# Optimization experiments

Hardware: AMD Instinct MI355X
Metric: run time of the kernel (lower is better)

Reference implementation:

```python
import jax, jax.numpy as jnp
import numpy as np

GROUP = 128          # quantization group size along K
ALIGN = 64           # M padding alignment (DeepGEMM, no swap-ab)
FP8_MAX = 448.0      # E4M3 max
EPS = 1e-4
MIN_SCALE = EPS / FP8_MAX


def _quant_per_token_group(a_bf16):
    """Per-token, per-128-group fp8 quantization along K.
    a_bf16: [M, K] bf16 -> (q [M, K] f32 fp8-rounded values, scales [M, K/GROUP] f32)"""
    M, K = a_bf16.shape
    g = a_bf16.astype(jnp.float32).reshape(M, K // GROUP, GROUP)
    amax = jnp.max(jnp.abs(g), axis=-1)                      # [M, K/GROUP]
    scale = jnp.maximum(amax, EPS) / FP8_MAX
    scale = jnp.maximum(scale, MIN_SCALE)                    # torch.clamp(min=...)
    q = jnp.clip(g / scale[..., None], -FP8_MAX, FP8_MAX)
    q = q.astype(jnp.float8_e4m3fn).astype(jnp.float32)      # fp8 rounding
    return q.reshape(M, K), scale


def setup_inputs() -> dict:
    key = jax.random.key(0)
    k1, k2, k3 = jax.random.split(key, 3)
    M, K, N = 8192, 4096, 4096
    inp = jax.random.normal(k1, (M, K), dtype=jnp.bfloat16)
    # weight stored as [N, K], values already fp8-representable (as DeepGEMM expects fp8 weights)
    w = jax.random.normal(k2, (N, K), dtype=jnp.float32)
    w = jnp.clip(w, -FP8_MAX, FP8_MAX).astype(jnp.float8_e4m3fn).astype(jnp.float32)
    # per-128x128-block weight scales, [N/128, K/128], positive
    ws = jax.random.uniform(k3, (N // GROUP, K // GROUP), dtype=jnp.float32,
                            minval=0.005, maxval=0.02)
    return {"input": inp, "weight": w, "weight_scales": ws}


def reference(input, weight, weight_scales):
    M, K = input.shape
    N = weight.shape[0]
    # pad M to multiple of ALIGN with zeros
    target_m = (M + ALIGN - 1) // ALIGN * ALIGN
    x = jnp.pad(input, ((0, target_m - M), (0, 0))) if target_m > M else input
    # fp8 per-token-group quantization of activations
    q, a_scales = _quant_per_token_group(x)                  # [Mp,K], [Mp,K/G]
    # dequantize both operands (the math fp8_gemm_nt computes)
    a_deq = q * jnp.repeat(a_scales, GROUP, axis=1)          # [Mp, K]
    w_deq = weight * jnp.repeat(jnp.repeat(weight_scales, GROUP, axis=0), GROUP, axis=1)  # [N, K]
    out = jnp.einsum('mk,nk->mn', a_deq, w_deq).astype(jnp.bfloat16)
    return out[:M, :]
```

## Files before the change

### kernel.cpp

```cpp
#include <hip/hip_runtime.h>
#include <hip/hip_bf16.h>

typedef unsigned short u16;
typedef unsigned int u32;
typedef __attribute__((ext_vector_type(8))) short short8;
typedef __attribute__((ext_vector_type(4))) float f32x4;

__device__ __forceinline__ u16 bf16_rne(float x) {
  __hip_bfloat16 h = __float2bfloat16(x);
  return __builtin_bit_cast(u16, h);
}

__global__ __launch_bounds__(256) void quant_dequant_a(
    const float* __restrict__ A, u16* __restrict__ AD, int K) {
  const int b = blockIdx.x;
  const int row = b >> 1;
  const int t = threadIdx.x;
  const size_t base = (size_t)row * K + (size_t)(b & 1) * 2048 + (size_t)t * 8;

  float4 v0 = *(const float4*)(A + base);
  float4 v1 = *(const float4*)(A + base + 4);
  float f[8] = {v0.x, v0.y, v0.z, v0.w, v1.x, v1.y, v1.z, v1.w};

  float am = 0.f;
#pragma unroll
  for (int i = 0; i < 8; ++i) am = fmaxf(am, fabsf(f[i]));
  am = fmaxf(am, __shfl_xor(am, 1));
  am = fmaxf(am, __shfl_xor(am, 2));
  am = fmaxf(am, __shfl_xor(am, 4));
  am = fmaxf(am, __shfl_xor(am, 8));
  const float scale = fmaxf(am, 1e-4f) / 448.0f;

  u16 o[8];
#pragma unroll
  for (int i = 0; i < 8; ++i) {
    float qv = fminf(fmaxf(f[i] / scale, -448.f), 448.f);
    int pk = __builtin_amdgcn_cvt_pk_fp8_f32(qv, qv, 0, false);
    float dv = __builtin_amdgcn_cvt_f32_fp8(pk, 0) * scale;
    o[i] = bf16_rne(dv);
  }
  *(uint4*)(AD + base) = *(const uint4*)o;
}

#define LSTR 72

__global__ __launch_bounds__(256, 2) void gemm_bf16_fused(
    const u16* __restrict__ AD, const float* __restrict__ Wf,
    const float* __restrict__ WS, u32* __restrict__ C32,
    int M, int N, int K) {
  __shared__ __align__(16) u16 As[128 * LSTR];
  __shared__ __align__(16) u16 Bs[128 * LSTR];

  const int NBN = N >> 7;
  const int bm = blockIdx.x / NBN;
  const int bn = blockIdx.x % NBN;

  const int tid = threadIdx.x, lane = tid & 63;
  const int wid = tid >> 6;
  const int wm = wid >> 1, wn = wid & 1;

  f32x4 acc[4][4];
#pragma unroll
  for (int mi = 0; mi < 4; ++mi)
#pragma unroll
    for (int ni = 0; ni < 4; ++ni)
      acc[mi][ni] = (f32x4){0.f, 0.f, 0.f, 0.f};

  const int KT = K >> 6;
  for (int g = 0; g < KT; ++g) {
    const float wsv = WS[bn * (K >> 7) + (g >> 1)];
    __syncthreads();
#pragma unroll
    for (int it = 0; it < 4; ++it) {
      const int ci = it * 256 + tid;
      const int r = ci >> 3, c = ci & 7;
      uint4 av = *(const uint4*)(AD + (size_t)(bm * 128 + r) * K + g * 64 + c * 8);
      *(uint4*)(As + r * LSTR + c * 8) = av;
      const float* bsrc = Wf + (size_t)(bn * 128 + r) * K + g * 64 + c * 8;
      float4 b0 = ((const float4*)bsrc)[0];
      float4 b1 = ((const float4*)bsrc)[1];
      u16 o[8];
      o[0] = bf16_rne(b0.x * wsv); o[1] = bf16_rne(b0.y * wsv);
      o[2] = bf16_rne(b0.z * wsv); o[3] = bf16_rne(b0.w * wsv);
      o[4] = bf16_rne(b1.x * wsv); o[5] = bf16_rne(b1.y * wsv);
      o[6] = bf16_rne(b1.z * wsv); o[7] = bf16_rne(b1.w * wsv);
      *(uint4*)(Bs + r * LSTR + c * 8) = *(const uint4*)o;
    }
    __syncthreads();

#pragma unroll
    for (int kk = 0; kk < 2; ++kk) {
      const int ko = kk * 32 + ((lane >> 4) << 3);
      short8 af[4], bfr[4];
#pragma unroll
      for (int mi = 0; mi < 4; ++mi) {
        const int rw = wm * 64 + mi * 16 + (lane & 15);
        af[mi] = *(const short8*)(As + rw * LSTR + ko);
      }
#pragma unroll
      for (int ni = 0; ni < 4; ++ni) {
        const int rw = wn * 64 + ni * 16 + (lane & 15);
        bfr[ni] = *(const short8*)(Bs + rw * LSTR + ko);
      }
#pragma unroll
      for (int mi = 0; mi < 4; ++mi)
#pragma unroll
        for (int ni = 0; ni < 4; ++ni)
          acc[mi][ni] = __builtin_amdgcn_mfma_f32_16x16x32_bf16(af[mi], bfr[ni], acc[mi][ni], 0, 0, 0);
    }
  }

  const int col = bn * 128 + wn * 64 + (lane & 15);
#pragma unroll
  for (int mi = 0; mi < 4; ++mi) {
#pragma unroll
    for (int j = 0; j < 4; ++j) {
      const size_t row = (size_t)(bm * 128 + wm * 64 + mi * 16 + ((lane >> 4) << 2) + j);
#pragma unroll
      for (int ni = 0; ni < 4; ++ni) {
        C32[row * N + col + ni * 16] = ((u32)bf16_rne(acc[mi][ni][j])) << 16;
      }
    }
  }
}

extern "C" void kernel_launch(void* const* d_in, const int* in_sizes, int n_in,
                              void* d_out, int out_size, void* d_ws, size_t ws_size,
                              hipStream_t stream) {
  const float* A = (const float*)d_in[0];
  const float* W = (const float*)d_in[1];
  const float* WS = (const float*)d_in[2];
  const int K = 4096, N = 4096;
  const int M = in_sizes[0] / K;

  u16* AD = (u16*)d_ws;

  quant_dequant_a<<<M * 2, 256, 0, stream>>>(A, AD, K);
  gemm_bf16_fused<<<(M / 128) * (N / 128), 256, 0, stream>>>(
      AD, W, WS, (u32*)d_out, M, N, K);
}
```

Baseline: 376.3 us.

## Replace GEMM with 256x256 LDS-DMA double-buffered kernel and separate weight dequant

Weight dequantization to bf16 moves out of the GEMM inner loop into a separate pre-pass kernel. The GEMM is rewritten with 256x256 tiles, 512 threads, direct global-to-LDS loads, XOR-swizzled LDS, double buffering, setprio around MFMA, and an XCD-aware block remap. Activation quant and GEMM are split into two M-halves so the workspace holds only half of A. This adds extra kernel launches and a full pass over W, in exchange for removing the per-tile float32 weight loads and conversions from the GEMM.

```diff
diff --git a/kernel.cpp b/kernel.cpp
--- a/kernel.cpp
+++ b/kernel.cpp
@@ -42,86 +42,143 @@
   *(uint4*)(AD + base) = *(const uint4*)o;
 }
 
-#define LSTR 72
-
-__global__ __launch_bounds__(256, 2) void gemm_bf16_fused(
-    const u16* __restrict__ AD, const float* __restrict__ Wf,
-    const float* __restrict__ WS, u32* __restrict__ C32,
-    int M, int N, int K) {
-  __shared__ __align__(16) u16 As[128 * LSTR];
-  __shared__ __align__(16) u16 Bs[128 * LSTR];
-
-  const int NBN = N >> 7;
-  const int bm = blockIdx.x / NBN;
-  const int bn = blockIdx.x % NBN;
-
-  const int tid = threadIdx.x, lane = tid & 63;
-  const int wid = tid >> 6;
-  const int wm = wid >> 1, wn = wid & 1;
-
-  f32x4 acc[4][4];
-#pragma unroll
-  for (int mi = 0; mi < 4; ++mi)
-#pragma unroll
-    for (int ni = 0; ni < 4; ++ni)
-      acc[mi][ni] = (f32x4){0.f, 0.f, 0.f, 0.f};
-
+__global__ __launch_bounds__(256) void dequant_w(
+    const float* __restrict__ W, const float* __restrict__ WS,
+    u16* __restrict__ WD, int K, int KG) {
+  const int b = blockIdx.x;
+  const int n = b >> 1;
+  const int t = threadIdx.x;
+  const int kof = (b & 1) * 2048 + t * 8;
+  const float ws = WS[(n >> 7) * KG + (kof >> 7)];
+  const size_t base = (size_t)n * K + kof;
+  float4 v0 = *(const float4*)(W + base);
+  float4 v1 = *(const float4*)(W + base + 4);
+  u16 o[8];
+  o[0] = bf16_rne(v0.x * ws); o[1] = bf16_rne(v0.y * ws);
+  o[2] = bf16_rne(v0.z * ws); o[3] = bf16_rne(v0.w * ws);
+  o[4] = bf16_rne(v1.x * ws); o[5] = bf16_rne(v1.y * ws);
+  o[6] = bf16_rne(v1.z * ws); o[7] = bf16_rne(v1.w * ws);
+  *(uint4*)(WD + base) = *(const uint4*)o;
+}
+
+#define GLDS16(g, l) __builtin_amdgcn_global_load_lds( \
+    (const __attribute__((address_space(1))) void*)(g), \
+    (__attribute__((address_space(3))) void*)(l), 16, 0, 0)
+
+#define STAGE2(TILE, R, BUF) do { \
+    GLDS16(A8 + (size_t)(arow0 + (R)*64 + srow) * rs + (size_t)(TILE)*128 + scs, \
+           sA + (BUF)*32768 + (R)*8192 + tid*16); \
+    GLDS16(B8 + (size_t)(brow0 + (R)*64 + srow) * rs + (size_t)(TILE)*128 + scs, \
+           sB + (BUF)*32768 + (R)*8192 + tid*16); \
+  } while (0)
+
+#define READ_A(H) \
+  _Pragma("unroll") for (int mi2 = 0; mi2 < 4; ++mi2) \
+    _Pragma("unroll") for (int kk = 0; kk < 2; ++kk) \
+      a[mi2][kk] = *(const short8*)(Ab + (rA0 + (H)*64 + mi2*16)*128 + \
+                                    ((((kk<<2)|kq)^swA)<<4));
+
+#define READ_B(NI0) \
+  _Pragma("unroll") for (int ni2 = 0; ni2 < 2; ++ni2) \
+    _Pragma("unroll") for (int kk = 0; kk < 2; ++kk) \
+      bfr[(NI0)+ni2][kk] = *(const short8*)(Bb + (rB0 + ((NI0)+ni2)*16)*128 + \
+                                            ((((kk<<2)|kq)^swB)<<4));
+
+#define MFMA_Q(MH, NH) do { \
+    __builtin_amdgcn_s_setprio(1); \
+    _Pragma("unroll") for (int mi2 = 0; mi2 < 4; ++mi2) \
+      _Pragma("unroll") for (int ni2 = 0; ni2 < 2; ++ni2) \
+        _Pragma("unroll") for (int kk = 0; kk < 2; ++kk) \
+          acc[(MH)*4+mi2][(NH)*2+ni2] = __builtin_amdgcn_mfma_f32_16x16x32_bf16( \
+              a[mi2][kk], bfr[(NH)*2+ni2][kk], acc[(MH)*4+mi2][(NH)*2+ni2], 0, 0, 0); \
+    __builtin_amdgcn_s_setprio(0); \
+  } while (0)
+
+__global__ __launch_bounds__(512, 2) void gemm_8p(
+    const u16* __restrict__ AD, const u16* __restrict__ WD,
+    u32* __restrict__ C32, int N, int K) {
+  __shared__ __align__(16) uint8_t smem[131072];
+  uint8_t* sA = smem;
+  uint8_t* sB = smem + 65536;
+
+  const int NBN = N >> 8;
+  int b = blockIdx.x;
+  const int per = gridDim.x >> 3;
+  b = (b & 7) * per + (b >> 3);
+  const int bm = b / NBN, bn = b % NBN;
+
+  const int tid = threadIdx.x, lane = tid & 63, wid = tid >> 6;
+  const int wm = wid >> 2, wn = wid & 3;
+
+  const uint8_t* A8 = (const uint8_t*)AD;
+  const uint8_t* B8 = (const uint8_t*)WD;
+  const size_t rs = (size_t)K * 2;
+
+  const int srow = tid >> 3;
+  const int sc   = tid & 7;
+  const int scs  = (sc ^ (srow & 7)) << 4;
+  const int arow0 = bm * 256;
+  const int brow0 = bn * 256;
+
+  const int rA0 = wm * 128 + (lane & 15);
+  const int rB0 = wn * 64 + (lane & 15);
+  const int kq  = lane >> 4;
+  const int swA = rA0 & 7, swB = rB0 & 7;
+
+  f32x4 acc[8][4];
+#pragma unroll
+  for (int i = 0; i < 8; ++i)
+#pragma unroll
+    for (int j = 0; j < 4; ++j) acc[i][j] = (f32x4){0.f, 0.f, 0.f, 0.f};
+
+#pragma unroll
+  for (int r = 0; r < 4; ++r) STAGE2(0, r, 0);
+  asm volatile("s_waitcnt vmcnt(0)" ::: "memory");
+  __builtin_amdgcn_s_barrier();
+
+  short8 a[4][2], bfr[4][2];
   const int KT = K >> 6;
-  for (int g = 0; g < KT; ++g) {
-    const float wsv = WS[bn * (K >> 7) + (g >> 1)];
-    __syncthreads();
-#pragma unroll
-    for (int it = 0; it < 4; ++it) {
-      const int ci = it * 256 + tid;
-      const int r = ci >> 3, c = ci & 7;
-      uint4 av = *(const uint4*)(AD + (size_t)(bm * 128 + r) * K + g * 64 + c * 8);
-      *(uint4*)(As + r * LSTR + c * 8) = av;
-      const float* bsrc = Wf + (size_t)(bn * 128 + r) * K + g * 64 + c * 8;
-      float4 b0 = ((const float4*)bsrc)[0];
-      float4 b1 = ((const float4*)bsrc)[1];
-      u16 o[8];
-      o[0] = bf16_rne(b0.x * wsv); o[1] = bf16_rne(b0.y * wsv);
-      o[2] = bf16_rne(b0.z * wsv); o[3] = bf16_rne(b0.w * wsv);
-      o[4] = bf16_rne(b1.x * wsv); o[5] = bf16_rne(b1.y * wsv);
-      o[6] = bf16_rne(b1.z * wsv); o[7] = bf16_rne(b1.w * wsv);
-      *(uint4*)(Bs + r * LSTR + c * 8) = *(const uint4*)o;
+
+  for (int kt = 0; kt < KT; ++kt) {
+    const int cur = kt & 1, nxt = cur ^ 1;
+    const bool more = (kt + 1 < KT);
+    const uint8_t* Ab = sA + cur * 32768;
+    const uint8_t* Bb = sB + cur * 32768;
+
+    if (more) STAGE2(kt + 1, 0, nxt);
+    READ_A(0)
+    READ_B(0)
+    MFMA_Q(0, 0);
+    __builtin_amdgcn_s_barrier();
+
+    if (more) STAGE2(kt + 1, 1, nxt);
+    READ_B(2)
+    MFMA_Q(0, 1);
+    __builtin_amdgcn_s_barrier();
+
+    if (more) STAGE2(kt + 1, 2, nxt);
+    READ_A(1)
+    MFMA_Q(1, 0);
+    __builtin_amdgcn_s_barrier();
+
+    if (more) STAGE2(kt + 1, 3, nxt);
+    MFMA_Q(1, 1);
+    __builtin_amdgcn_sched_barrier(0);
+    asm volatile("s_waitcnt vmcnt(0)" ::: "memory");
+    __builtin_amdgcn_s_barrier();
+  }
+
+  const int c0 = bn * 256 + wn * 64 + (lane & 15);
+  const int r0q = bm * 256 + wm * 128 + ((lane >> 4) << 2);
+#pragma unroll
+  for (int mi = 0; mi < 8; ++mi)
+#pragma unroll
+    for (int j = 0; j < 4; ++j) {
+      const size_t row = (size_t)(r0q + mi * 16 + j);
+#pragma unroll
+      for (int ni = 0; ni < 4; ++ni)
+        C32[row * N + c0 + ni * 16] = ((u32)bf16_rne(acc[mi][ni][j])) << 16;
     }
-    __syncthreads();
-
-#pragma unroll
-    for (int kk = 0; kk < 2; ++kk) {
-      const int ko = kk * 32 + ((lane >> 4) << 3);
-      short8 af[4], bfr[4];
-#pragma unroll
-      for (int mi = 0; mi < 4; ++mi) {
-        const int rw = wm * 64 + mi * 16 + (lane & 15);
-        af[mi] = *(const short8*)(As + rw * LSTR + ko);
-      }
-#pragma unroll
-      for (int ni = 0; ni < 4; ++ni) {
-        const int rw = wn * 64 + ni * 16 + (lane & 15);
-        bfr[ni] = *(const short8*)(Bs + rw * LSTR + ko);
-      }
-#pragma unroll
-      for (int mi = 0; mi < 4; ++mi)
-#pragma unroll
-        for (int ni = 0; ni < 4; ++ni)
-          acc[mi][ni] = __builtin_amdgcn_mfma_f32_16x16x32_bf16(af[mi], bfr[ni], acc[mi][ni], 0, 0, 0);
-    }
-  }
-
-  const int col = bn * 128 + wn * 64 + (lane & 15);
-#pragma unroll
-  for (int mi = 0; mi < 4; ++mi) {
-#pragma unroll
-    for (int j = 0; j < 4; ++j) {
-      const size_t row = (size_t)(bm * 128 + wm * 64 + mi * 16 + ((lane >> 4) << 2) + j);
-#pragma unroll
-      for (int ni = 0; ni < 4; ++ni) {
-        C32[row * N + col + ni * 16] = ((u32)bf16_rne(acc[mi][ni][j])) << 16;
-      }
-    }
-  }
 }
 
 extern "C" void kernel_launch(void* const* d_in, const int* in_sizes, int n_in,
@@ -132,10 +189,18 @@
   const float* WS = (const float*)d_in[2];
   const int K = 4096, N = 4096;
   const int M = in_sizes[0] / K;
-
-  u16* AD = (u16*)d_ws;
-
-  quant_dequant_a<<<M * 2, 256, 0, stream>>>(A, AD, K);
-  gemm_bf16_fused<<<(M / 128) * (N / 128), 256, 0, stream>>>(
-      AD, W, WS, (u32*)d_out, M, N, K);
-}
+  const int Mh = M / 2;
+
+  u16* ADh = (u16*)d_ws;
+  u16* WDp = ADh + (size_t)Mh * K;
+  u32* C = (u32*)d_out;
+
+  dequant_w<<<N * 2, 256, 0, stream>>>(W, WS, WDp, K, K / 128);
+
+  quant_dequant_a<<<Mh * 2, 256, 0, stream>>>(A, ADh, K);
+  gemm_8p<<<(Mh / 256) * (N / 256), 512, 0, stream>>>(ADh, WDp, C, N, K);
+
+  quant_dequant_a<<<Mh * 2, 256, 0, stream>>>(A + (size_t)Mh * K, ADh, K);
+  gemm_8p<<<(Mh / 256) * (N / 256), 512, 0, stream>>>(ADh, WDp,
+                                                      C + (size_t)Mh * N, N, K);
+}
```

New measurement: 301.4 us. 1.25x faster.
